# Optimization experiments

Hardware: AMD Instinct MI355X
Metric: run time of the kernel (lower is better)

The kernel has to match this reference:

```python
import jax, jax.numpy as jnp
import numpy as np

N = 8192
IN_C, HID_C, OUT_C = 128, 256, 128


def setup_inputs() -> dict:
    key = jax.random.key(0)
    ks = jax.random.split(key, 6)
    return {
        "x": jax.random.normal(ks[0], (N, IN_C), dtype=jnp.float32),
        "adaptive_params": jax.random.normal(ks[1], (N, N), dtype=jnp.float32),
        "W1": jax.random.normal(ks[2], (IN_C, HID_C), dtype=jnp.float32) * (1.0 / np.sqrt(IN_C)),
        "b1": jax.random.normal(ks[3], (HID_C,), dtype=jnp.float32) * 0.01,
        "W2": jax.random.normal(ks[4], (HID_C, OUT_C), dtype=jnp.float32) * (1.0 / np.sqrt(HID_C)),
        "b2": jax.random.normal(ks[5], (OUT_C,), dtype=jnp.float32) * 0.01,
    }


def _normalized_adj(adaptive_params):
    # initial_adj = I; A = sigmoid(sym(I + P)) where sym(M) = (M + M^T)/2
    n = adaptive_params.shape[0]
    eye = jnp.eye(n, dtype=adaptive_params.dtype)
    sym = eye + 0.5 * (adaptive_params + adaptive_params.T)
    A = jax.nn.sigmoid(sym)
    # sigmoid > 0 everywhere -> edge_index covers all N^2 pairs (dense graph).
    # PyG gcn_norm (add_self_loops=True, fill_value=1.0): A_hat = A + I,
    # then symmetric degree normalization D^-1/2 A_hat D^-1/2.
    A_hat = A + eye
    dinv = jax.lax.rsqrt(jnp.sum(A_hat, axis=1))  # [N]
    return A_hat * dinv[:, None] * dinv[None, :]


def reference(x, adaptive_params, W1, b1, W2, b2):
    A_norm = _normalized_adj(adaptive_params)          # [N, N]
    h = jax.nn.relu(A_norm @ (x @ W1) + b1)            # [N, HID_C]
    out = A_norm @ (h @ W2) + b2                       # [N, OUT_C]
    return out
```

## Files before the change

### kernel.cpp

```cpp
#include <hip/hip_runtime.h>
#include <hip/hip_bf16.h>
#include <cstdint>

typedef unsigned short u16;
typedef unsigned short u16x4 __attribute__((ext_vector_type(4)));
typedef unsigned short u16x8 __attribute__((ext_vector_type(8)));
typedef _Float16 f16x8 __attribute__((ext_vector_type(8)));
typedef float f32x4 __attribute__((ext_vector_type(4)));

constexpr int NN   = 8192;
constexpr int INC  = 128;
constexpr int HIDC = 256;
constexpr int OUTC = 128;
constexpr int KSPLIT = 8;

__device__ __forceinline__ u16 f2h(float f) {
    _Float16 h = (_Float16)f;
    return __builtin_bit_cast(u16, h);
}
__device__ __forceinline__ float h2f(u16 u) {
    return (float)__builtin_bit_cast(_Float16, u);
}
__device__ __forceinline__ float fast_sigmoid(float z) {
    float e;
    asm("v_exp_f32 %0, %1" : "=v"(e) : "v"(z * -1.44269504088896f));
    float s;
    asm("v_rcp_f32 %0, %1" : "=v"(s) : "v"(1.0f + e));
    return s;
}

typedef __attribute__((address_space(1))) const void* gptr_t;
typedef __attribute__((address_space(3))) void* sptr_t;
#define GLD16(g, s) __builtin_amdgcn_global_load_lds((gptr_t)(g), (sptr_t)(s), 16, 0, 0)

__global__ __launch_bounds__(512, 4) void k_adj(const float* __restrict__ P,
                                                u16* __restrict__ AH,
                                                float* __restrict__ rowsum,
                                                const float* __restrict__ W2,
                                                u16* __restrict__ W2T) {
    const int t = threadIdx.x;
    if (blockIdx.x == 0) {
        for (int e = t; e < OUTC * HIDC; e += 512) {
            int c = e >> 8, k = e & 255;
            W2T[c * HIDC + k] = f2h(W2[k * OUTC + c]);
        }
        return;
    }
    int bid = blockIdx.x - 1;
    int bi, bj;
    if (bid >= 2016)      { bi = bj = bid - 2016; }
    else if (bid >= 1984) { bi = 31; bj = 32 + (bid - 1984); }
    else {
        int u = bid >> 6, v = bid & 63;
        if (v < 63 - u) { bi = u;      bj = u + 1 + v; }
        else            { bi = 62 - u; bj = v; }
    }
    constexpr int LW = 136;
    __shared__ u16 hB[128 * LW];
    __shared__ float cs[8][128];
    const int i0 = bi * 128, j0 = bj * 128;
    const bool diag = (bi == bj);

    #pragma unroll
    for (int p = 0; p < 4; ++p) {
        int idx = p * 512 + t;
        int r = idx >> 4, m = idx & 15;
        const float* pb = P + (size_t)(j0 + r) * NN + i0 + m * 8;
        f32x4 b0 = __builtin_nontemporal_load((const f32x4*)pb);
        f32x4 b1 = __builtin_nontemporal_load((const f32x4*)(pb + 4));
        u16x8 hb;
        hb[0] = f2h(b0[0]); hb[1] = f2h(b0[1]); hb[2] = f2h(b0[2]); hb[3] = f2h(b0[3]);
        hb[4] = f2h(b1[0]); hb[5] = f2h(b1[1]); hb[6] = f2h(b1[2]); hb[7] = f2h(b1[3]);
        int pos = m ^ ((r >> 3) & 7);
        *(u16x8*)&hB[r * LW + pos * 8] = hb;
    }

    const int rb = t >> 4, cb = t & 15;
    const int R = rb * 4, C = cb * 8;
    f32x4 a0[4], a1[4];
    #pragma unroll
    for (int i = 0; i < 4; ++i) {
        const float* pa = P + (size_t)(i0 + R + i) * NN + j0 + C;
        a0[i] = __builtin_nontemporal_load((const f32x4*)pa);
        a1[i] = __builtin_nontemporal_load((const f32x4*)(pa + 4));
    }
    __syncthreads();

    float rsum[4] = {0.f, 0.f, 0.f, 0.f};
    float csum[8] = {0.f, 0.f, 0.f, 0.f, 0.f, 0.f, 0.f, 0.f};
    u16x4 mir[8];
    {
        u16x4 bv[8];
        #pragma unroll
        for (int j = 0; j < 8; ++j) {
            int r = C + j;
            int pos = (rb >> 1) ^ (cb & 7);
            bv[j] = *(const u16x4*)&hB[r * LW + pos * 8 + (rb & 1) * 4];
        }
        #pragma unroll
        for (int i = 0; i < 4; ++i) {
            u16x8 o;
            #pragma unroll
            for (int j = 0; j < 8; ++j) {
                float av = (j < 4) ? a0[i][j] : a1[i][j - 4];
                float z = 0.5f * (av + h2f(bv[j][i]));
                bool dg = (i0 + R + i) == (j0 + C + j);
                if (dg) z += 1.0f;
                float s = fast_sigmoid(z);
                if (dg) s += 1.0f;
                u16 h = f2h(s);
                o[j] = h;
                mir[j][i] = h;
                rsum[i] += s;
                csum[j] += s;
            }
            *(u16x8*)(AH + (size_t)(i0 + R + i) * NN + j0 + C) = o;
        }
        if (!diag) {
            #pragma unroll
            for (int j = 0; j < 8; ++j) {
                int r = C + j;
                int pos = (rb >> 1) ^ (cb & 7);
                *(u16x4*)&hB[r * LW + pos * 8 + (rb & 1) * 4] = mir[j];
            }
        }
    }

    #pragma unroll
    for (int m = 1; m <= 8; m <<= 1) {
        #pragma unroll
        for (int i = 0; i < 4; ++i) rsum[i] += __shfl_xor(rsum[i], m);
    }
    if (cb == 0) {
        #pragma unroll
        for (int i = 0; i < 4; ++i) atomicAdd(&rowsum[i0 + R + i], rsum[i]);
    }

    if (!diag) {
        #pragma unroll
        for (int j = 0; j < 8; ++j) {
            csum[j] += __shfl_xor(csum[j], 16);
            csum[j] += __shfl_xor(csum[j], 32);
        }
        const int w = t >> 6;
        if ((t & 48) == 0) {
            #pragma unroll
            for (int j = 0; j < 8; ++j) cs[w][C + j] = csum[j];
        }
    }
    __syncthreads();

    if (!diag) {
        const int r2 = t >> 4, m = t & 15;
        #pragma unroll
        for (int p = 0; p < 4; ++p) {
            int rr = r2 + p * 32;
            int pos = m ^ ((rr >> 3) & 7);
            *(u16x8*)(AH + (size_t)(j0 + rr) * NN + i0 + m * 8) =
                *(const u16x8*)&hB[rr * LW + pos * 8];
        }
        if (t < 128) {
            float s = 0.f;
            #pragma unroll
            for (int k = 0; k < 8; ++k) s += cs[k][t];
            atomicAdd(&rowsum[j0 + t], s);
        }
    }
}

__global__ __launch_bounds__(256) void k_xw1(const float* __restrict__ x,
                                             const float* __restrict__ W1,
                                             const float* __restrict__ rowsum,
                                             u16* __restrict__ XW1T) {
    const int t = threadIdx.x;
    __shared__ float xs[32 * 129];
    const int i0 = blockIdx.x * 32;
    #pragma unroll
    for (int p = 0; p < 4; ++p) {
        int idx = p * 256 + t;
        int r = idx >> 5, c4 = idx & 31;
        f32x4 v = __builtin_nontemporal_load(
            (const f32x4*)(x + (size_t)(i0 + r) * INC + c4 * 4));
        int o = r * 129 + c4 * 4;
        xs[o] = v[0]; xs[o + 1] = v[1]; xs[o + 2] = v[2]; xs[o + 3] = v[3];
    }
    __syncthreads();
    const int i = t & 31, g = t >> 5;
    const float di = 1.0f / sqrtf(rowsum[i0 + i]);
    #pragma unroll
    for (int p = 0; p < 2; ++p) {
        const int cbase = g * 32 + p * 16;
        float acc[16];
        #pragma unroll
        for (int cc = 0; cc < 16; ++cc) acc[cc] = 0.f;
        for (int k = 0; k < 128; ++k) {
            float xv = xs[i * 129 + k];
            const float4* wr4 = reinterpret_cast<const float4*>(W1 + k * HIDC + cbase);
            float4 w0 = wr4[0], w1 = wr4[1], w2 = wr4[2], w3 = wr4[3];
            acc[0]  = fmaf(xv, w0.x, acc[0]);  acc[1]  = fmaf(xv, w0.y, acc[1]);
            acc[2]  = fmaf(xv, w0.z, acc[2]);  acc[3]  = fmaf(xv, w0.w, acc[3]);
            acc[4]  = fmaf(xv, w1.x, acc[4]);  acc[5]  = fmaf(xv, w1.y, acc[5]);
            acc[6]  = fmaf(xv, w1.z, acc[6]);  acc[7]  = fmaf(xv, w1.w, acc[7]);
            acc[8]  = fmaf(xv, w2.x, acc[8]);  acc[9]  = fmaf(xv, w2.y, acc[9]);
            acc[10] = fmaf(xv, w2.z, acc[10]); acc[11] = fmaf(xv, w2.w, acc[11]);
            acc[12] = fmaf(xv, w3.x, acc[12]); acc[13] = fmaf(xv, w3.y, acc[13]);
            acc[14] = fmaf(xv, w3.z, acc[14]); acc[15] = fmaf(xv, w3.w, acc[15]);
        }
        #pragma unroll
        for (int cc = 0; cc < 16; ++cc)
            XW1T[(size_t)(cbase + cc) * NN + i0 + i] = f2h(di * acc[cc]);
    }
}

#define PH_MID() do { __builtin_amdgcn_s_barrier();                             \
    asm volatile("s_waitcnt lgkmcnt(0)" ::: "memory");                          \
    __builtin_amdgcn_sched_barrier(0);                                          \
    __builtin_amdgcn_s_setprio(1); } while (0)

#define PH_NW() do { __builtin_amdgcn_s_setprio(0);                             \
    __builtin_amdgcn_s_barrier(); } while (0)

#define PH_W() do { __builtin_amdgcn_s_setprio(0);                              \
    if constexpr (BN == 256) { asm volatile("s_waitcnt vmcnt(6)" ::: "memory"); } \
    else                     { asm volatile("s_waitcnt vmcnt(4)" ::: "memory"); } \
    __builtin_amdgcn_s_barrier(); } while (0)

#define PH_W0() do { __builtin_amdgcn_s_setprio(0);                             \
    asm volatile("s_waitcnt vmcnt(0)" ::: "memory");                            \
    __builtin_amdgcn_s_barrier(); } while (0)

template <int BN>
__global__ __launch_bounds__(512, 2) void k_gemm8(const u16* __restrict__ A,
                                                  const u16* __restrict__ BT,
                                                  u16* __restrict__ partial) {
    constexpr int NI = BN / 128;
    constexpr int NQB = BN / 64;
    constexpr int BUFB = BN * 128;
    constexpr int KCH = NN / KSPLIT;
    constexpr int NT = KCH / 64;
    constexpr int ITER = NT / 2;
    __shared__ __align__(16) char lds[65536 + 2 * BUFB];

    const int t = threadIdx.x;
    const int l = t & 63, w = t >> 6;
    const int wr = w >> 2, wc = w & 3;
    const int g2 = (blockIdx.x & 7) * 32 + (blockIdx.x >> 3);
    const int m0 = (g2 & 31) * 256;
    const int kc = g2 >> 5;
    const int kbase = kc * KCH;

    const int D16 = t * 16;
    const int Ds = D16 ^ (((D16 >> 7) & 7) << 4);
    const int rS = Ds >> 7, cS = (Ds & 127) >> 1;

    f32x4 acc[8][NI * 2];
    #pragma unroll
    for (int i = 0; i < 8; ++i)
        #pragma unroll
        for (int j = 0; j < NI * 2; ++j) acc[i][j] = {0.f, 0.f, 0.f, 0.f};

    f16x8 a[4][2];
    f16x8 bf[2][NI][2];

    auto stageA = [&](int b, int q, int tile) {
        GLD16(A + (size_t)(m0 + q * 64 + rS) * NN + kbase + tile * 64 + cS,
              &lds[b * 32768 + q * 8192 + D16]);
    };
    auto stageB = [&](int b, int q, int tile) {
        GLD16(BT + (size_t)(q * 64 + rS) * NN + kbase + tile * 64 + cS,
              &lds[65536 + b * BUFB + q * 8192 + D16]);
    };
    auto readA = [&](int b, int mh) {
        #pragma unroll
        for (int mi = 0; mi < 4; ++mi)
            #pragma unroll
            for (int s = 0; s < 2; ++s) {
                int r = wr * 128 + mh * 64 + mi * 16 + (l & 15);
                a[mi][s] = *(const f16x8*)&lds[b * 32768 + r * 128 +
                    ((s * 64 + ((l >> 4) * 16)) ^ ((r & 7) << 4))];
            }
    };
    auto readB = [&](int b, int nh) {
        #pragma unroll
        for (int ni = 0; ni < NI; ++ni)
            #pragma unroll
            for (int s = 0; s < 2; ++s) {
                int r = wc * (BN / 4) + nh * (NI * 16) + ni * 16 + (l & 15);
                bf[nh][ni][s] = *(const f16x8*)&lds[65536 + b * BUFB + r * 128 +
                    ((s * 64 + ((l >> 4) * 16)) ^ ((r & 7) << 4))];
            }
    };
    auto mfmaq = [&](int mh, int nh) {
        #pragma unroll
        for (int s = 0; s < 2; ++s)
            #pragma unroll
            for (int mi = 0; mi < 4; ++mi)
                #pragma unroll
                for (int ni = 0; ni < NI; ++ni)
                    acc[mh * 4 + mi][nh * NI + ni] =
                        __builtin_amdgcn_mfma_f32_16x16x32_f16(a[mi][s], bf[nh][ni][s],
                            acc[mh * 4 + mi][nh * NI + ni], 0, 0, 0);
    };

    #pragma unroll
    for (int q = 0; q < NQB; ++q) stageB(0, q, 0);
    #pragma unroll
    for (int q = 0; q < 4; ++q) stageA(0, q, 0);
    #pragma unroll
    for (int q = 0; q < NQB; ++q) stageB(1, q, 1);
    stageA(1, 0, 1); stageA(1, 1, 1);
    if constexpr (BN == 256) { asm volatile("s_waitcnt vmcnt(6)" ::: "memory"); }
    else                     { asm volatile("s_waitcnt vmcnt(4)" ::: "memory"); }
    __builtin_amdgcn_s_barrier();

    for (int it = 0; it < ITER - 1; ++it) {
        const int TP = 2 * it + 1, TE = 2 * it + 2, TO = 2 * it + 3;
        readA(0, 0); readB(0, 0); stageA(1, 2, TP); stageA(1, 3, TP);
        PH_MID(); mfmaq(0, 0); PH_NW();
        readB(0, 1);
        PH_MID(); mfmaq(0, 1); PH_NW();
        readA(0, 1); stageB(0, 0, TE); stageB(0, 1, TE);
        PH_MID(); mfmaq(1, 0); PH_NW();
        if constexpr (BN == 256) { stageB(0, 2, TE); stageB(0, 3, TE); }
        stageA(0, 0, TE); stageA(0, 1, TE);
        PH_MID(); mfmaq(1, 1); PH_W();
        readA(1, 0); readB(1, 0); stageA(0, 2, TE); stageA(0, 3, TE);
        PH_MID(); mfmaq(0, 0); PH_NW();
        readB(1, 1);
        PH_MID(); mfmaq(0, 1); PH_NW();
        readA(1, 1); stageB(1, 0, TO); stageB(1, 1, TO);
        PH_MID(); mfmaq(1, 0); PH_NW();
        if constexpr (BN == 256) { stageB(1, 2, TO); stageB(1, 3, TO); }
        stageA(1, 0, TO); stageA(1, 1, TO);
        PH_MID(); mfmaq(1, 1); PH_W();
    }
    readA(0, 0); readB(0, 0); stageA(1, 2, NT - 1); stageA(1, 3, NT - 1);
    PH_MID(); mfmaq(0, 0); PH_NW();
    readB(0, 1);
    PH_MID(); mfmaq(0, 1); PH_NW();
    readA(0, 1);
    PH_MID(); mfmaq(1, 0); PH_NW();
    PH_MID(); mfmaq(1, 1); PH_W0();
    readA(1, 0); readB(1, 0);
    PH_MID(); mfmaq(0, 0); PH_NW();
    readB(1, 1);
    PH_MID(); mfmaq(0, 1); PH_NW();
    readA(1, 1);
    PH_MID(); mfmaq(1, 0); PH_NW();
    PH_MID(); mfmaq(1, 1);
    __builtin_amdgcn_s_setprio(0);

    u16* pout = partial + (size_t)kc * NN * BN;
    #pragma unroll
    for (int mh = 0; mh < 2; ++mh)
        #pragma unroll
        for (int mi = 0; mi < 4; ++mi)
            #pragma unroll
            for (int j = 0; j < 4; ++j) {
                int grow = m0 + wr * 128 + mh * 64 + mi * 16 + (l >> 4) * 4 + j;
                #pragma unroll
                for (int nh = 0; nh < 2; ++nh)
                    #pragma unroll
                    for (int ni = 0; ni < NI; ++ni) {
                        int gcol = wc * (BN / 4) + nh * (NI * 16) + ni * 16 + (l & 15);
                        pout[(size_t)grow * BN + gcol] = f2h(acc[mh * 4 + mi][nh * NI + ni][j]);
                    }
            }
}

__global__ __launch_bounds__(512) void k_epi1hw2m(const u16* __restrict__ partial,
                                                  const float* __restrict__ rowsum,
                                                  const float* __restrict__ b1,
                                                  const u16* __restrict__ W2T,
                                                  u16* __restrict__ HW2T) {
    __shared__ __align__(16) char lds[81920];
    const int t = threadIdx.x;
    const int l = t & 63, w = t >> 6;
    const int i0 = blockIdx.x * 32;

    #pragma unroll
    for (int p = 0; p < 8; ++p) {
        int D = (p * 512 + t) * 16;
        int row = D >> 9;
        int col = (D & 511) ^ ((row & 7) << 4);
        GLD16(W2T + (size_t)row * HIDC + (col >> 1), &lds[D]);
    }
    #pragma unroll
    for (int p = 0; p < 2; ++p) {
        int qi = p * 512 + t;
        int i = qi >> 5, cq = qi & 31;
        float s[8] = {0.f, 0.f, 0.f, 0.f, 0.f, 0.f, 0.f, 0.f};
        #pragma unroll
        for (int kc = 0; kc < KSPLIT; ++kc) {
            u16x8 pv = __builtin_nontemporal_load(
                (const u16x8*)(partial + ((size_t)kc * NN + i0 + i) * HIDC + cq * 8));
            #pragma unroll
            for (int k = 0; k < 8; ++k) s[k] += h2f(pv[k]);
        }
        const float di = 1.0f / sqrtf(rowsum[i0 + i]);
        u16x8 o;
        #pragma unroll
        for (int k = 0; k < 8; ++k)
            o[k] = f2h(di * fmaxf(fmaf(di, s[k], b1[cq * 8 + k]), 0.f));
        *(u16x8*)&lds[65536 + i * 512 + ((cq * 16) ^ ((i & 7) << 4))] = o;
    }
    asm volatile("s_waitcnt vmcnt(0)" ::: "memory");
    __syncthreads();

    const int wm = w >> 1, wn = w & 1;
    f32x4 acc[2];
    acc[0] = {0.f, 0.f, 0.f, 0.f}; acc[1] = {0.f, 0.f, 0.f, 0.f};
    for (int kt = 0; kt < 8; ++kt) {
        f16x8 av[2], bv;
        const int cb2 = kt * 64 + (l >> 4) * 16;
        #pragma unroll
        for (int mi = 0; mi < 2; ++mi) {
            int r = wm * 32 + mi * 16 + (l & 15);
            av[mi] = *(const f16x8*)&lds[r * 512 + (cb2 ^ ((r & 7) << 4))];
        }
        {
            int ri = wn * 16 + (l & 15);
            bv = *(const f16x8*)&lds[65536 + ri * 512 + (cb2 ^ ((ri & 7) << 4))];
        }
        #pragma unroll
        for (int mi = 0; mi < 2; ++mi)
            acc[mi] = __builtin_amdgcn_mfma_f32_16x16x32_f16(av[mi], bv, acc[mi], 0, 0, 0);
    }
    #pragma unroll
    for (int mi = 0; mi < 2; ++mi)
        #pragma unroll
        for (int j = 0; j < 4; ++j) {
            int c = wm * 32 + mi * 16 + (l >> 4) * 4 + j;
            int ic = wn * 16 + (l & 15);
            HW2T[(size_t)c * NN + i0 + ic] = f2h(acc[mi][j]);
        }
}

__global__ __launch_bounds__(256) void k_epi2(const u16* __restrict__ partial,
                                              const float* __restrict__ rowsum,
                                              const float* __restrict__ b2,
                                              float* __restrict__ out) {
    const int idx = blockIdx.x * 256 + threadIdx.x;
    const int i = idx >> 4, cq = idx & 15;
    float s[8] = {0.f, 0.f, 0.f, 0.f, 0.f, 0.f, 0.f, 0.f};
    #pragma unroll
    for (int kc = 0; kc < KSPLIT; ++kc) {
        u16x8 pv = __builtin_nontemporal_load(
            (const u16x8*)(partial + ((size_t)kc * NN + i) * OUTC + cq * 8));
        #pragma unroll
        for (int k = 0; k < 8; ++k) s[k] += h2f(pv[k]);
    }
    const float di = 1.0f / sqrtf(rowsum[i]);
    float o[8];
    #pragma unroll
    for (int k = 0; k < 8; ++k) o[k] = fmaf(di, s[k], b2[cq * 8 + k]);
    float* op = out + (size_t)i * OUTC + cq * 8;
    *reinterpret_cast<float4*>(op) = make_float4(o[0], o[1], o[2], o[3]);
    *reinterpret_cast<float4*>(op + 4) = make_float4(o[4], o[5], o[6], o[7]);
}

extern "C" void kernel_launch(void* const* d_in, const int* in_sizes, int n_in,
                              void* d_out, int out_size, void* d_ws, size_t ws_size,
                              hipStream_t stream) {
    const float* x  = (const float*)d_in[0];
    const float* P  = (const float*)d_in[1];
    const float* W1 = (const float*)d_in[2];
    const float* b1 = (const float*)d_in[3];
    const float* W2 = (const float*)d_in[4];
    const float* b2 = (const float*)d_in[5];
    float* out = (float*)d_out;
    char* ws = (char*)d_ws;

    u16*   AH      = (u16*)(ws);
    u16*   XW1T    = (u16*)(ws + 134217728ull);
    u16*   W2T     = (u16*)(ws + 138412032ull);
    u16*   HW2T    = (u16*)(ws + 138477568ull);
    float* rowsum  = (float*)(ws + 140574720ull);
    u16*   partial = (u16*)(ws + 140607488ull);

    hipMemsetAsync(rowsum, 0, NN * sizeof(float), stream);
    k_adj<<<2081, 512, 0, stream>>>(P, AH, rowsum, W2, W2T);
    k_xw1<<<256, 256, 0, stream>>>(x, W1, rowsum, XW1T);
    k_gemm8<HIDC><<<256, 512, 0, stream>>>(AH, XW1T, partial);
    k_epi1hw2m<<<256, 512, 0, stream>>>(partial, rowsum, b1, W2T, HW2T);
    k_gemm8<OUTC><<<256, 512, 0, stream>>>(AH, HW2T, partial);
    k_epi2<<<512, 256, 0, stream>>>(partial, rowsum, b2, out);
}
```

Baseline: 203.6 us.

## Fold x@W1 into adjacency kernel and stage GEMM partial stores through LDS

The unscaled x@W1 product now runs as extra blocks inside the adjacency kernel, so it overlaps with the bandwidth-bound adjacency pass. A small elementwise kernel then applies the degree scaling and fp16 conversion once the row sums are complete. Separately, the GEMM epilogue writes its partial results to swizzled LDS and then copies them out as 16-byte row-contiguous stores, replacing the scattered 2-byte global stores. The cost is an extra fp32 intermediate buffer, one extra launch, and added LDS round trips and barriers in the GEMM epilogue.

```diff
diff --git a/kernel.cpp b/kernel.cpp
--- a/kernel.cpp
+++ b/kernel.cpp
@@ -37,8 +37,14 @@
                                                 u16* __restrict__ AH,
                                                 float* __restrict__ rowsum,
                                                 const float* __restrict__ W2,
-                                                u16* __restrict__ W2T) {
+                                                u16* __restrict__ W2T,
+                                                const float* __restrict__ x,
+                                                const float* __restrict__ W1,
+                                                float* __restrict__ XW1R) {
     const int t = threadIdx.x;
+    __shared__ __align__(16) u16 hB[128 * 136];
+    __shared__ float cs[8][128];
+
     if (blockIdx.x == 0) {
         for (int e = t; e < OUTC * HIDC; e += 512) {
             int c = e >> 8, k = e & 255;
@@ -46,6 +52,43 @@
         }
         return;
     }
+    if (blockIdx.x >= 2081) {
+        float* xs = (float*)hB;
+        const int i0 = (blockIdx.x - 2081) * 32;
+        #pragma unroll
+        for (int p = 0; p < 2; ++p) {
+            int idx = p * 512 + t;
+            int r = idx >> 5, c4 = idx & 31;
+            f32x4 v = __builtin_nontemporal_load(
+                (const f32x4*)(x + (size_t)(i0 + r) * INC + c4 * 4));
+            int o = r * 129 + c4 * 4;
+            xs[o] = v[0]; xs[o + 1] = v[1]; xs[o + 2] = v[2]; xs[o + 3] = v[3];
+        }
+        __syncthreads();
+        const int i = t & 31, g = t >> 5;
+        const int cbase = g * 16;
+        float acc[16];
+        #pragma unroll
+        for (int cc = 0; cc < 16; ++cc) acc[cc] = 0.f;
+        for (int k = 0; k < 128; ++k) {
+            float xv = xs[i * 129 + k];
+            const float4* wr4 = reinterpret_cast<const float4*>(W1 + k * HIDC + cbase);
+            float4 w0 = wr4[0], w1 = wr4[1], w2 = wr4[2], w3 = wr4[3];
+            acc[0]  = fmaf(xv, w0.x, acc[0]);  acc[1]  = fmaf(xv, w0.y, acc[1]);
+            acc[2]  = fmaf(xv, w0.z, acc[2]);  acc[3]  = fmaf(xv, w0.w, acc[3]);
+            acc[4]  = fmaf(xv, w1.x, acc[4]);  acc[5]  = fmaf(xv, w1.y, acc[5]);
+            acc[6]  = fmaf(xv, w1.z, acc[6]);  acc[7]  = fmaf(xv, w1.w, acc[7]);
+            acc[8]  = fmaf(xv, w2.x, acc[8]);  acc[9]  = fmaf(xv, w2.y, acc[9]);
+            acc[10] = fmaf(xv, w2.z, acc[10]); acc[11] = fmaf(xv, w2.w, acc[11]);
+            acc[12] = fmaf(xv, w3.x, acc[12]); acc[13] = fmaf(xv, w3.y, acc[13]);
+            acc[14] = fmaf(xv, w3.z, acc[14]); acc[15] = fmaf(xv, w3.w, acc[15]);
+        }
+        #pragma unroll
+        for (int cc = 0; cc < 16; ++cc)
+            XW1R[(size_t)(cbase + cc) * NN + i0 + i] = acc[cc];
+        return;
+    }
+
     int bid = blockIdx.x - 1;
     int bi, bj;
     if (bid >= 2016)      { bi = bj = bid - 2016; }
@@ -56,8 +99,6 @@
         else            { bi = 62 - u; bj = v; }
     }
     constexpr int LW = 136;
-    __shared__ u16 hB[128 * LW];
-    __shared__ float cs[8][128];
     const int i0 = bi * 128, j0 = bj * 128;
     const bool diag = (bi == bj);
 
@@ -168,48 +209,21 @@
     }
 }
 
-__global__ __launch_bounds__(256) void k_xw1(const float* __restrict__ x,
-                                             const float* __restrict__ W1,
-                                             const float* __restrict__ rowsum,
-                                             u16* __restrict__ XW1T) {
-    const int t = threadIdx.x;
-    __shared__ float xs[32 * 129];
-    const int i0 = blockIdx.x * 32;
-    #pragma unroll
-    for (int p = 0; p < 4; ++p) {
-        int idx = p * 256 + t;
-        int r = idx >> 5, c4 = idx & 31;
-        f32x4 v = __builtin_nontemporal_load(
-            (const f32x4*)(x + (size_t)(i0 + r) * INC + c4 * 4));
-        int o = r * 129 + c4 * 4;
-        xs[o] = v[0]; xs[o + 1] = v[1]; xs[o + 2] = v[2]; xs[o + 3] = v[3];
-    }
-    __syncthreads();
-    const int i = t & 31, g = t >> 5;
-    const float di = 1.0f / sqrtf(rowsum[i0 + i]);
-    #pragma unroll
-    for (int p = 0; p < 2; ++p) {
-        const int cbase = g * 32 + p * 16;
-        float acc[16];
-        #pragma unroll
-        for (int cc = 0; cc < 16; ++cc) acc[cc] = 0.f;
-        for (int k = 0; k < 128; ++k) {
-            float xv = xs[i * 129 + k];
-            const float4* wr4 = reinterpret_cast<const float4*>(W1 + k * HIDC + cbase);
-            float4 w0 = wr4[0], w1 = wr4[1], w2 = wr4[2], w3 = wr4[3];
-            acc[0]  = fmaf(xv, w0.x, acc[0]);  acc[1]  = fmaf(xv, w0.y, acc[1]);
-            acc[2]  = fmaf(xv, w0.z, acc[2]);  acc[3]  = fmaf(xv, w0.w, acc[3]);
-            acc[4]  = fmaf(xv, w1.x, acc[4]);  acc[5]  = fmaf(xv, w1.y, acc[5]);
-            acc[6]  = fmaf(xv, w1.z, acc[6]);  acc[7]  = fmaf(xv, w1.w, acc[7]);
-            acc[8]  = fmaf(xv, w2.x, acc[8]);  acc[9]  = fmaf(xv, w2.y, acc[9]);
-            acc[10] = fmaf(xv, w2.z, acc[10]); acc[11] = fmaf(xv, w2.w, acc[11]);
-            acc[12] = fmaf(xv, w3.x, acc[12]); acc[13] = fmaf(xv, w3.y, acc[13]);
-            acc[14] = fmaf(xv, w3.z, acc[14]); acc[15] = fmaf(xv, w3.w, acc[15]);
-        }
-        #pragma unroll
-        for (int cc = 0; cc < 16; ++cc)
-            XW1T[(size_t)(cbase + cc) * NN + i0 + i] = f2h(di * acc[cc]);
-    }
+__global__ __launch_bounds__(256) void k_scale(const float* __restrict__ XW1R,
+                                               const float* __restrict__ rowsum,
+                                               u16* __restrict__ XW1T) {
+    const int idx = blockIdx.x * 256 + threadIdx.x;
+    const int c = idx >> 10;
+    const int io = (idx & 1023) * 8;
+    const float* src = XW1R + (size_t)c * NN + io;
+    f32x4 v0 = *(const f32x4*)src, v1 = *(const f32x4*)(src + 4);
+    f32x4 r0 = *(const f32x4*)(rowsum + io), r1 = *(const f32x4*)(rowsum + io + 4);
+    u16x8 o;
+    o[0] = f2h(v0[0] / sqrtf(r0[0])); o[1] = f2h(v0[1] / sqrtf(r0[1]));
+    o[2] = f2h(v0[2] / sqrtf(r0[2])); o[3] = f2h(v0[3] / sqrtf(r0[3]));
+    o[4] = f2h(v1[0] / sqrtf(r1[0])); o[5] = f2h(v1[1] / sqrtf(r1[1]));
+    o[6] = f2h(v1[2] / sqrtf(r1[2])); o[7] = f2h(v1[3] / sqrtf(r1[3]));
+    *(u16x8*)(XW1T + (size_t)c * NN + io) = o;
 }
 
 #define PH_MID() do { __builtin_amdgcn_s_barrier();                             \
@@ -350,22 +364,36 @@
     PH_MID(); mfmaq(1, 1);
     __builtin_amdgcn_s_setprio(0);
 
-    u16* pout = partial + (size_t)kc * NN * BN;
+    __syncthreads();
+    u16* cl = (u16*)lds;
     #pragma unroll
     for (int mh = 0; mh < 2; ++mh)
         #pragma unroll
         for (int mi = 0; mi < 4; ++mi)
             #pragma unroll
             for (int j = 0; j < 4; ++j) {
-                int grow = m0 + wr * 128 + mh * 64 + mi * 16 + (l >> 4) * 4 + j;
+                int lr = wr * 128 + mh * 64 + mi * 16 + (l >> 4) * 4 + j;
+                int swz = ((lr >> 2) & 3) << 4;
                 #pragma unroll
                 for (int nh = 0; nh < 2; ++nh)
                     #pragma unroll
                     for (int ni = 0; ni < NI; ++ni) {
-                        int gcol = wc * (BN / 4) + nh * (NI * 16) + ni * 16 + (l & 15);
-                        pout[(size_t)grow * BN + gcol] = f2h(acc[mh * 4 + mi][nh * NI + ni][j]);
+                        int c = wc * (BN / 4) + nh * (NI * 16) + ni * 16 + (l & 15);
+                        cl[lr * BN + (c ^ swz)] = f2h(acc[mh * 4 + mi][nh * NI + ni][j]);
                     }
             }
+    __syncthreads();
+    u16* pout = partial + (size_t)kc * NN * BN;
+    constexpr int CPR = BN / 8;
+    constexpr int PASS = 256 * CPR / 512;
+    #pragma unroll
+    for (int p = 0; p < PASS; ++p) {
+        int idx = p * 512 + t;
+        int lr = idx / CPR, ch = idx % CPR;
+        int chs = ch ^ (((lr >> 2) & 3) << 1);
+        u16x8 v = *(const u16x8*)&cl[lr * BN + chs * 8];
+        *(u16x8*)(pout + (size_t)(m0 + lr) * BN + ch * 8) = v;
+    }
 }
 
 __global__ __launch_bounds__(512) void k_epi1hw2m(const u16* __restrict__ partial,
@@ -477,10 +505,11 @@
     u16*   HW2T    = (u16*)(ws + 138477568ull);
     float* rowsum  = (float*)(ws + 140574720ull);
     u16*   partial = (u16*)(ws + 140607488ull);
+    float* XW1R    = (float*)(ws + 174161920ull);
 
     hipMemsetAsync(rowsum, 0, NN * sizeof(float), stream);
-    k_adj<<<2081, 512, 0, stream>>>(P, AH, rowsum, W2, W2T);
-    k_xw1<<<256, 256, 0, stream>>>(x, W1, rowsum, XW1T);
+    k_adj<<<2337, 512, 0, stream>>>(P, AH, rowsum, W2, W2T, x, W1, XW1R);
+    k_scale<<<1024, 256, 0, stream>>>(XW1R, rowsum, XW1T);
     k_gemm8<HIDC><<<256, 512, 0, stream>>>(AH, XW1T, partial);
     k_epi1hw2m<<<256, 512, 0, stream>>>(partial, rowsum, b1, W2T, HW2T);
     k_gemm8<OUTC><<<256, 512, 0, stream>>>(AH, HW2T, partial);
```

New measurement: 216.0 us. +6.1%, slower.

## Fuse post-adjacency stages into one cooperative kernel with grid syncs

Applied to the files above, without the earlier changes.

Replaces the five kernels after the adjacency build (XW1, first GEMM, epilogue+HW2, second GEMM, final epilogue) with a single cooperative kernel of 256 blocks. Stages are separated by grid-wide syncs and share a 128 KB LDS buffer. The goal is to remove the per-launch overhead and drain/fill gaps between dependent kernels. In exchange it adds grid-sync cost, and the larger static LDS with launch_bounds(512,2) may limit occupancy or fail cooperative residency. The XW1 stage now runs 512 threads per block, each computing one 16-column slice.

```diff
diff --git a/kernel.cpp b/kernel.cpp
--- a/kernel.cpp
+++ b/kernel.cpp
@@ -1,6 +1,9 @@
 #include <hip/hip_runtime.h>
 #include <hip/hip_bf16.h>
+#include <hip/hip_cooperative_groups.h>
 #include <cstdint>
+
+namespace cg = cooperative_groups;
 
 typedef unsigned short u16;
 typedef unsigned short u16x4 __attribute__((ext_vector_type(4)));
@@ -168,50 +171,6 @@
     }
 }
 
-__global__ __launch_bounds__(256) void k_xw1(const float* __restrict__ x,
-                                             const float* __restrict__ W1,
-                                             const float* __restrict__ rowsum,
-                                             u16* __restrict__ XW1T) {
-    const int t = threadIdx.x;
-    __shared__ float xs[32 * 129];
-    const int i0 = blockIdx.x * 32;
-    #pragma unroll
-    for (int p = 0; p < 4; ++p) {
-        int idx = p * 256 + t;
-        int r = idx >> 5, c4 = idx & 31;
-        f32x4 v = __builtin_nontemporal_load(
-            (const f32x4*)(x + (size_t)(i0 + r) * INC + c4 * 4));
-        int o = r * 129 + c4 * 4;
-        xs[o] = v[0]; xs[o + 1] = v[1]; xs[o + 2] = v[2]; xs[o + 3] = v[3];
-    }
-    __syncthreads();
-    const int i = t & 31, g = t >> 5;
-    const float di = 1.0f / sqrtf(rowsum[i0 + i]);
-    #pragma unroll
-    for (int p = 0; p < 2; ++p) {
-        const int cbase = g * 32 + p * 16;
-        float acc[16];
-        #pragma unroll
-        for (int cc = 0; cc < 16; ++cc) acc[cc] = 0.f;
-        for (int k = 0; k < 128; ++k) {
-            float xv = xs[i * 129 + k];
-            const float4* wr4 = reinterpret_cast<const float4*>(W1 + k * HIDC + cbase);
-            float4 w0 = wr4[0], w1 = wr4[1], w2 = wr4[2], w3 = wr4[3];
-            acc[0]  = fmaf(xv, w0.x, acc[0]);  acc[1]  = fmaf(xv, w0.y, acc[1]);
-            acc[2]  = fmaf(xv, w0.z, acc[2]);  acc[3]  = fmaf(xv, w0.w, acc[3]);
-            acc[4]  = fmaf(xv, w1.x, acc[4]);  acc[5]  = fmaf(xv, w1.y, acc[5]);
-            acc[6]  = fmaf(xv, w1.z, acc[6]);  acc[7]  = fmaf(xv, w1.w, acc[7]);
-            acc[8]  = fmaf(xv, w2.x, acc[8]);  acc[9]  = fmaf(xv, w2.y, acc[9]);
-            acc[10] = fmaf(xv, w2.z, acc[10]); acc[11] = fmaf(xv, w2.w, acc[11]);
-            acc[12] = fmaf(xv, w3.x, acc[12]); acc[13] = fmaf(xv, w3.y, acc[13]);
-            acc[14] = fmaf(xv, w3.z, acc[14]); acc[15] = fmaf(xv, w3.w, acc[15]);
-        }
-        #pragma unroll
-        for (int cc = 0; cc < 16; ++cc)
-            XW1T[(size_t)(cbase + cc) * NN + i0 + i] = f2h(di * acc[cc]);
-    }
-}
-
 #define PH_MID() do { __builtin_amdgcn_s_barrier();                             \
     asm volatile("s_waitcnt lgkmcnt(0)" ::: "memory");                          \
     __builtin_amdgcn_sched_barrier(0);                                          \
@@ -230,21 +189,20 @@
     __builtin_amdgcn_s_barrier(); } while (0)
 
 template <int BN>
-__global__ __launch_bounds__(512, 2) void k_gemm8(const u16* __restrict__ A,
-                                                  const u16* __restrict__ BT,
-                                                  u16* __restrict__ partial) {
+__device__ __forceinline__ void gemm_body(const u16* __restrict__ A,
+                                          const u16* __restrict__ BT,
+                                          u16* __restrict__ partial,
+                                          char* lds, int blk, int t) {
     constexpr int NI = BN / 128;
     constexpr int NQB = BN / 64;
     constexpr int BUFB = BN * 128;
     constexpr int KCH = NN / KSPLIT;
     constexpr int NT = KCH / 64;
     constexpr int ITER = NT / 2;
-    __shared__ __align__(16) char lds[65536 + 2 * BUFB];
-
-    const int t = threadIdx.x;
+
     const int l = t & 63, w = t >> 6;
     const int wr = w >> 2, wc = w & 3;
-    const int g2 = (blockIdx.x & 7) * 32 + (blockIdx.x >> 3);
+    const int g2 = (blk & 7) * 32 + (blk >> 3);
     const int m0 = (g2 & 31) * 256;
     const int kc = g2 >> 5;
     const int kbase = kc * KCH;
@@ -368,95 +326,147 @@
             }
 }
 
-__global__ __launch_bounds__(512) void k_epi1hw2m(const u16* __restrict__ partial,
+__global__ __launch_bounds__(512, 2) void k_fused(const float* __restrict__ x,
+                                                  const float* __restrict__ W1,
                                                   const float* __restrict__ rowsum,
+                                                  u16* __restrict__ XW1T,
+                                                  const u16* __restrict__ AH,
+                                                  u16* __restrict__ partial,
                                                   const float* __restrict__ b1,
                                                   const u16* __restrict__ W2T,
-                                                  u16* __restrict__ HW2T) {
-    __shared__ __align__(16) char lds[81920];
+                                                  u16* __restrict__ HW2T,
+                                                  const float* __restrict__ b2,
+                                                  float* __restrict__ out) {
+    cg::grid_group grid = cg::this_grid();
+    __shared__ __align__(16) char lds[131072];
     const int t = threadIdx.x;
+    const int bid = blockIdx.x;
     const int l = t & 63, w = t >> 6;
-    const int i0 = blockIdx.x * 32;
-
-    #pragma unroll
-    for (int p = 0; p < 8; ++p) {
-        int D = (p * 512 + t) * 16;
-        int row = D >> 9;
-        int col = (D & 511) ^ ((row & 7) << 4);
-        GLD16(W2T + (size_t)row * HIDC + (col >> 1), &lds[D]);
-    }
-    #pragma unroll
-    for (int p = 0; p < 2; ++p) {
-        int qi = p * 512 + t;
-        int i = qi >> 5, cq = qi & 31;
+
+    {
+        float* xs = (float*)lds;
+        const int i0 = bid * 32;
+        #pragma unroll
+        for (int p = 0; p < 2; ++p) {
+            int idx = p * 512 + t;
+            int r = idx >> 5, c4 = idx & 31;
+            f32x4 v = __builtin_nontemporal_load(
+                (const f32x4*)(x + (size_t)(i0 + r) * INC + c4 * 4));
+            int o = r * 129 + c4 * 4;
+            xs[o] = v[0]; xs[o + 1] = v[1]; xs[o + 2] = v[2]; xs[o + 3] = v[3];
+        }
+        __syncthreads();
+        const int i = t & 31, g = t >> 5;
+        const int cbase = g * 16;
+        const float di = 1.0f / sqrtf(rowsum[i0 + i]);
+        float acc[16];
+        #pragma unroll
+        for (int cc = 0; cc < 16; ++cc) acc[cc] = 0.f;
+        for (int k = 0; k < 128; ++k) {
+            float xv = xs[i * 129 + k];
+            const float4* wr4 = reinterpret_cast<const float4*>(W1 + k * HIDC + cbase);
+            float4 w0 = wr4[0], w1 = wr4[1], w2 = wr4[2], w3 = wr4[3];
+            acc[0]  = fmaf(xv, w0.x, acc[0]);  acc[1]  = fmaf(xv, w0.y, acc[1]);
+            acc[2]  = fmaf(xv, w0.z, acc[2]);  acc[3]  = fmaf(xv, w0.w, acc[3]);
+            acc[4]  = fmaf(xv, w1.x, acc[4]);  acc[5]  = fmaf(xv, w1.y, acc[5]);
+            acc[6]  = fmaf(xv, w1.z, acc[6]);  acc[7]  = fmaf(xv, w1.w, acc[7]);
+            acc[8]  = fmaf(xv, w2.x, acc[8]);  acc[9]  = fmaf(xv, w2.y, acc[9]);
+            acc[10] = fmaf(xv, w2.z, acc[10]); acc[11] = fmaf(xv, w2.w, acc[11]);
+            acc[12] = fmaf(xv, w3.x, acc[12]); acc[13] = fmaf(xv, w3.y, acc[13]);
+            acc[14] = fmaf(xv, w3.z, acc[14]); acc[15] = fmaf(xv, w3.w, acc[15]);
+        }
+        #pragma unroll
+        for (int cc = 0; cc < 16; ++cc)
+            XW1T[(size_t)(cbase + cc) * NN + i0 + i] = f2h(di * acc[cc]);
+    }
+    grid.sync();
+
+    gemm_body<HIDC>(AH, XW1T, partial, lds, bid, t);
+    grid.sync();
+
+    {
+        const int i0 = bid * 32;
+        #pragma unroll
+        for (int p = 0; p < 8; ++p) {
+            int D = (p * 512 + t) * 16;
+            int row = D >> 9;
+            int col = (D & 511) ^ ((row & 7) << 4);
+            GLD16(W2T + (size_t)row * HIDC + (col >> 1), &lds[D]);
+        }
+        #pragma unroll
+        for (int p = 0; p < 2; ++p) {
+            int qi = p * 512 + t;
+            int i = qi >> 5, cq = qi & 31;
+            float s[8] = {0.f, 0.f, 0.f, 0.f, 0.f, 0.f, 0.f, 0.f};
+            #pragma unroll
+            for (int kc = 0; kc < KSPLIT; ++kc) {
+                u16x8 pv = __builtin_nontemporal_load(
+                    (const u16x8*)(partial + ((size_t)kc * NN + i0 + i) * HIDC + cq * 8));
+                #pragma unroll
+                for (int k = 0; k < 8; ++k) s[k] += h2f(pv[k]);
+            }
+            const float di = 1.0f / sqrtf(rowsum[i0 + i]);
+            u16x8 o;
+            #pragma unroll
+            for (int k = 0; k < 8; ++k)
+                o[k] = f2h(di * fmaxf(fmaf(di, s[k], b1[cq * 8 + k]), 0.f));
+            *(u16x8*)&lds[65536 + i * 512 + ((cq * 16) ^ ((i & 7) << 4))] = o;
+        }
+        asm volatile("s_waitcnt vmcnt(0)" ::: "memory");
+        __syncthreads();
+
+        const int wm = w >> 1, wn = w & 1;
+        f32x4 acc[2];
+        acc[0] = {0.f, 0.f, 0.f, 0.f}; acc[1] = {0.f, 0.f, 0.f, 0.f};
+        for (int kt = 0; kt < 8; ++kt) {
+            f16x8 av[2], bv;
+            const int cb2 = kt * 64 + (l >> 4) * 16;
+            #pragma unroll
+            for (int mi = 0; mi < 2; ++mi) {
+                int r = wm * 32 + mi * 16 + (l & 15);
+                av[mi] = *(const f16x8*)&lds[r * 512 + (cb2 ^ ((r & 7) << 4))];
+            }
+            {
+                int ri = wn * 16 + (l & 15);
+                bv = *(const f16x8*)&lds[65536 + ri * 512 + (cb2 ^ ((ri & 7) << 4))];
+            }
+            #pragma unroll
+            for (int mi = 0; mi < 2; ++mi)
+                acc[mi] = __builtin_amdgcn_mfma_f32_16x16x32_f16(av[mi], bv, acc[mi], 0, 0, 0);
+        }
+        #pragma unroll
+        for (int mi = 0; mi < 2; ++mi)
+            #pragma unroll
+            for (int j = 0; j < 4; ++j) {
+                int c = wm * 32 + mi * 16 + (l >> 4) * 4 + j;
+                int ic = wn * 16 + (l & 15);
+                HW2T[(size_t)c * NN + i0 + ic] = f2h(acc[mi][j]);
+            }
+    }
+    grid.sync();
+
+    gemm_body<OUTC>(AH, HW2T, partial, lds, bid, t);
+    grid.sync();
+
+    {
+        const int idx = bid * 512 + t;
+        const int i = idx >> 4, cq = idx & 15;
         float s[8] = {0.f, 0.f, 0.f, 0.f, 0.f, 0.f, 0.f, 0.f};
         #pragma unroll
         for (int kc = 0; kc < KSPLIT; ++kc) {
             u16x8 pv = __builtin_nontemporal_load(
-                (const u16x8*)(partial + ((size_t)kc * NN + i0 + i) * HIDC + cq * 8));
+                (const u16x8*)(partial + ((size_t)kc * NN + i) * OUTC + cq * 8));
             #pragma unroll
             for (int k = 0; k < 8; ++k) s[k] += h2f(pv[k]);
         }
-        const float di = 1.0f / sqrtf(rowsum[i0 + i]);
-        u16x8 o;
-        #pragma unroll
-        for (int k = 0; k < 8; ++k)
-            o[k] = f2h(di * fmaxf(fmaf(di, s[k], b1[cq * 8 + k]), 0.f));
-        *(u16x8*)&lds[65536 + i * 512 + ((cq * 16) ^ ((i & 7) << 4))] = o;
-    }
-    asm volatile("s_waitcnt vmcnt(0)" ::: "memory");
-    __syncthreads();
-
-    const int wm = w >> 1, wn = w & 1;
-    f32x4 acc[2];
-    acc[0] = {0.f, 0.f, 0.f, 0.f}; acc[1] = {0.f, 0.f, 0.f, 0.f};
-    for (int kt = 0; kt < 8; ++kt) {
-        f16x8 av[2], bv;
-        const int cb2 = kt * 64 + (l >> 4) * 16;
-        #pragma unroll
-        for (int mi = 0; mi < 2; ++mi) {
-            int r = wm * 32 + mi * 16 + (l & 15);
-            av[mi] = *(const f16x8*)&lds[r * 512 + (cb2 ^ ((r & 7) << 4))];
-        }
-        {
-            int ri = wn * 16 + (l & 15);
-            bv = *(const f16x8*)&lds[65536 + ri * 512 + (cb2 ^ ((ri & 7) << 4))];
-        }
-        #pragma unroll
-        for (int mi = 0; mi < 2; ++mi)
-            acc[mi] = __builtin_amdgcn_mfma_f32_16x16x32_f16(av[mi], bv, acc[mi], 0, 0, 0);
-    }
-    #pragma unroll
-    for (int mi = 0; mi < 2; ++mi)
-        #pragma unroll
-        for (int j = 0; j < 4; ++j) {
-            int c = wm * 32 + mi * 16 + (l >> 4) * 4 + j;
-            int ic = wn * 16 + (l & 15);
-            HW2T[(size_t)c * NN + i0 + ic] = f2h(acc[mi][j]);
-        }
-}
-
-__global__ __launch_bounds__(256) void k_epi2(const u16* __restrict__ partial,
-                                              const float* __restrict__ rowsum,
-                                              const float* __restrict__ b2,
-                                              float* __restrict__ out) {
-    const int idx = blockIdx.x * 256 + threadIdx.x;
-    const int i = idx >> 4, cq = idx & 15;
-    float s[8] = {0.f, 0.f, 0.f, 0.f, 0.f, 0.f, 0.f, 0.f};
-    #pragma unroll
-    for (int kc = 0; kc < KSPLIT; ++kc) {
-        u16x8 pv = __builtin_nontemporal_load(
-            (const u16x8*)(partial + ((size_t)kc * NN + i) * OUTC + cq * 8));
-        #pragma unroll
-        for (int k = 0; k < 8; ++k) s[k] += h2f(pv[k]);
-    }
-    const float di = 1.0f / sqrtf(rowsum[i]);
-    float o[8];
-    #pragma unroll
-    for (int k = 0; k < 8; ++k) o[k] = fmaf(di, s[k], b2[cq * 8 + k]);
-    float* op = out + (size_t)i * OUTC + cq * 8;
-    *reinterpret_cast<float4*>(op) = make_float4(o[0], o[1], o[2], o[3]);
-    *reinterpret_cast<float4*>(op + 4) = make_float4(o[4], o[5], o[6], o[7]);
+        const float di = 1.0f / sqrtf(rowsum[i]);
+        float o[8];
+        #pragma unroll
+        for (int k = 0; k < 8; ++k) o[k] = fmaf(di, s[k], b2[cq * 8 + k]);
+        float* op = out + (size_t)i * OUTC + cq * 8;
+        *reinterpret_cast<float4*>(op) = make_float4(o[0], o[1], o[2], o[3]);
+        *reinterpret_cast<float4*>(op + 4) = make_float4(o[4], o[5], o[6], o[7]);
+    }
 }
 
 extern "C" void kernel_launch(void* const* d_in, const int* in_sizes, int n_in,
@@ -480,9 +490,10 @@
 
     hipMemsetAsync(rowsum, 0, NN * sizeof(float), stream);
     k_adj<<<2081, 512, 0, stream>>>(P, AH, rowsum, W2, W2T);
-    k_xw1<<<256, 256, 0, stream>>>(x, W1, rowsum, XW1T);
-    k_gemm8<HIDC><<<256, 512, 0, stream>>>(AH, XW1T, partial);
-    k_epi1hw2m<<<256, 512, 0, stream>>>(partial, rowsum, b1, W2T, HW2T);
-    k_gemm8<OUTC><<<256, 512, 0, stream>>>(AH, HW2T, partial);
-    k_epi2<<<512, 256, 0, stream>>>(partial, rowsum, b2, out);
-}
+
+    void* args[] = {(void*)&x, (void*)&W1, (void*)&rowsum, (void*)&XW1T,
+                    (void*)&AH, (void*)&partial, (void*)&b1, (void*)&W2T,
+                    (void*)&HW2T, (void*)&b2, (void*)&out};
+    hipLaunchCooperativeKernel((const void*)k_fused, dim3(256), dim3(512),
+                               args, 0, stream);
+}
```

Measured after the change: 335.0 us. 1.65x slower.
